# Optimization experiments

Hardware: AMD Instinct MI355X
Metric: run time of the kernel (lower is better)

## Reference

```python
import jax, jax.numpy as jnp
import numpy as np

B, L, E, H = 4, 2048, 1024, 16
D = E // H  # head_dim = 64

def setup_inputs() -> dict:
    key = jax.random.key(0)
    ks = jax.random.split(key, 8)
    s = 1.0 / np.sqrt(E)
    return {
        "x_q": jax.random.normal(ks[0], (B, L, E), jnp.float32),
        "x_k": jax.random.normal(ks[1], (B, L, E), jnp.float32),
        "x_v": jax.random.normal(ks[2], (B, L, E), jnp.float32),
        "Wq": jax.random.uniform(ks[3], (E, E), jnp.float32, -s, s),
        "Wk": jax.random.uniform(ks[4], (E, E), jnp.float32, -s, s),
        "Wv": jax.random.uniform(ks[5], (E, E), jnp.float32, -s, s),
        "Wo": jax.random.uniform(ks[6], (E, E), jnp.float32, -s, s),
        "bo": jax.random.uniform(ks[7], (E,), jnp.float32, -s, s),
    }

def reference(x_q, x_k, x_v, Wq, Wk, Wv, Wo, bo):
    # projections (torch Linear: y = x @ W.T)
    Q = (x_q @ Wq.T).reshape(B, L, H, D).transpose(0, 2, 1, 3)  # (B,H,Lq,D)
    K = (x_k @ Wk.T).reshape(B, L, H, D).transpose(0, 2, 1, 3)
    V = (x_v @ Wv.T).reshape(B, L, H, D).transpose(0, 2, 1, 3)
    scale = 1.0 / jnp.sqrt(jnp.asarray(D, Q.dtype))
    scores = jnp.einsum('bhqd,bhkd->bhqk', Q, K) * scale  # (B,H,Lq,Lk)
    attn = jax.nn.softmax(scores, axis=-1)
    ctx = jnp.einsum('bhqk,bhkd->bhqd', attn, V)
    ctx = ctx.transpose(0, 2, 1, 3).reshape(B, L, E)
    return ctx @ Wo.T + bo
```

## Files before the change

### kernel.cpp

```cpp
#include <hip/hip_runtime.h>
#include <hip/hip_bf16.h>
#include <stdint.h>

typedef __bf16 bf16;
typedef __attribute__((ext_vector_type(8))) __bf16 bf16x8;
typedef __attribute__((ext_vector_type(4))) __bf16 bf16x4;
typedef __attribute__((ext_vector_type(4))) float f32x4;
typedef __attribute__((ext_vector_type(16))) float f32x16;
typedef __attribute__((ext_vector_type(4))) unsigned int u32x4;

#define MFMA(a, b, c) __builtin_amdgcn_mfma_f32_16x16x32_bf16(a, b, c, 0, 0, 0)
#define MFMA32(a, b, c) __builtin_amdgcn_mfma_f32_32x32x16_bf16(a, b, c, 0, 0, 0)

__device__ __forceinline__ void gload16(const void* g, void* l) {
  __builtin_amdgcn_global_load_lds(
      (const __attribute__((address_space(1))) void*)g,
      (__attribute__((address_space(3))) void*)l, 16, 0, 0);
}

__global__ void cvt4(const float* __restrict__ s0, const float* __restrict__ s1,
                     const float* __restrict__ s2, const float* __restrict__ s3,
                     bf16* __restrict__ d0, bf16* __restrict__ d1,
                     bf16* __restrict__ d2, bf16* __restrict__ d3, long n) {
  const float* s = blockIdx.y == 0 ? s0 : blockIdx.y == 1 ? s1 : blockIdx.y == 2 ? s2 : s3;
  bf16* d       = blockIdx.y == 0 ? d0 : blockIdx.y == 1 ? d1 : blockIdx.y == 2 ? d2 : d3;
  long i0 = ((long)blockIdx.x * blockDim.x + threadIdx.x) * 8;
  long gs = (long)gridDim.x * blockDim.x * 8;
  for (long i = i0; i < n; i += gs) {
    float4 a = *(const float4*)(s + i);
    float4 b = *(const float4*)(s + i + 4);
    bf16x8 ov;
    ov[0] = (bf16)a.x; ov[1] = (bf16)a.y; ov[2] = (bf16)a.z; ov[3] = (bf16)a.w;
    ov[4] = (bf16)b.x; ov[5] = (bf16)b.y; ov[6] = (bf16)b.z; ov[7] = (bf16)b.w;
    *(bf16x8*)(d + i) = ov;
  }
}

__device__ __forceinline__ void gemm_body(const bf16* __restrict__ A,
                                          const bf16* __restrict__ W,
                                          void* __restrict__ Cout,
                                          const float* __restrict__ bias,
                                          float scale, int mode,
                                          bf16* As, bf16* Bs) {
  const int tid = threadIdx.x;
  const int l = tid & 63, w = tid >> 6;
  const int lr = l & 15, lg = l >> 4;
  const int lin = blockIdx.y * 8 + blockIdx.x;
  const int nl = (lin & 7) * 64 + (lin >> 3);
  const int m0 = (nl >> 3) * 128, n0 = (nl & 7) * 128;
  const int wm = w >> 1, wn = w & 1;
  f32x4 acc[4][4];
  for (int i = 0; i < 4; i++)
    for (int j = 0; j < 4; j++)
      for (int r = 0; r < 4; r++) acc[i][j][r] = 0.f;

  auto STAGE = [&](int kt, int buf) {
#pragma unroll
    for (int i = 0; i < 2; i++) {
      int c = i * 256 + tid;
      int row = c >> 2, ch = c & 3;
      int sc = (ch ^ ((row >> 1) & 3)) * 8;
      gload16(A + (long)(m0 + row) * 1024 + kt + sc, (char*)As + buf * 8192 + c * 16);
      gload16(W + (long)(n0 + row) * 1024 + kt + sc, (char*)Bs + buf * 8192 + c * 16);
    }
  };

  STAGE(0, 0); STAGE(32, 1); STAGE(64, 2);

  for (int t = 0; t < 32; t++) {
    if (t <= 29)      asm volatile("s_waitcnt vmcnt(8) lgkmcnt(0)" ::: "memory");
    else if (t == 30) asm volatile("s_waitcnt vmcnt(4) lgkmcnt(0)" ::: "memory");
    else              asm volatile("s_waitcnt vmcnt(0) lgkmcnt(0)" ::: "memory");
    __builtin_amdgcn_s_barrier();
    __builtin_amdgcn_sched_barrier(0);
    const char* Ac = (const char*)As + (t & 3) * 8192;
    const char* Bc = (const char*)Bs + (t & 3) * 8192;
    bf16x8 af[4], bw[4];
#pragma unroll
    for (int i = 0; i < 4; i++) {
      int row = wm * 64 + i * 16 + lr;
      af[i] = *(const bf16x8*)(Ac + row * 64 + ((lg ^ ((row >> 1) & 3)) << 4));
    }
#pragma unroll
    for (int j = 0; j < 4; j++) {
      int row = wn * 64 + j * 16 + lr;
      bw[j] = *(const bf16x8*)(Bc + row * 64 + ((lg ^ ((row >> 1) & 3)) << 4));
    }
#pragma unroll
    for (int i = 0; i < 4; i++)
#pragma unroll
      for (int j = 0; j < 4; j++)
        acc[i][j] = MFMA(af[i], bw[j], acc[i][j]);
    if (t <= 28) STAGE((t + 3) * 32, (t + 3) & 3);
  }

  for (int i = 0; i < 4; i++)
    for (int j = 0; j < 4; j++) {
      int row = m0 + wm * 64 + i * 16 + lg * 4;
      int col = n0 + wn * 64 + j * 16 + lr;
      f32x4 v = acc[i][j];
      if (mode == 2) {
        float* O = (float*)Cout;
        float bb = bias[col];
        for (int r = 0; r < 4; r++) O[(long)(row + r) * 1024 + col] = v[r] + bb;
      } else if (mode == 0) {
        bf16* O = (bf16*)Cout;
        for (int r = 0; r < 4; r++) {
          int rr = row + r;
          long idx = ((long)((rr >> 11) * 16 + (col >> 6)) * 2048 + (rr & 2047)) * 64 + (col & 63);
          O[idx] = (bf16)(v[r] * scale);
        }
      } else {
        bf16* O = (bf16*)Cout;
        long idx = ((long)((row >> 11) * 16 + (col >> 6)) * 64 + (col & 63)) * 2048 + (row & 2047);
        bf16x4 pk;
        for (int r = 0; r < 4; r++) pk[r] = (bf16)v[r];
        *(bf16x4*)(O + idx) = pk;
      }
    }
}

__global__ __launch_bounds__(256) void gemm_qkv(const bf16* __restrict__ Xb,
                                                const bf16* __restrict__ Wb,
                                                bf16* __restrict__ Ob,
                                                float qscale) {
  __shared__ bf16 As[4][128 * 32];
  __shared__ bf16 Bs[4][128 * 32];
  const int z = blockIdx.z;
  const bf16* A = Xb + (long)z * 8192 * 1024;
  const bf16* W = Wb + (long)z * 1024 * 1024;
  bf16* O = Ob + (long)z * 8192 * 1024;
  const float scale = (z == 0) ? qscale : 1.0f;
  const int mode = (z == 2) ? 1 : 0;
  gemm_body(A, W, O, nullptr, scale, mode, &As[0][0], &Bs[0][0]);
}

__global__ __launch_bounds__(256) void gemm_out(const bf16* __restrict__ A,
                                                const bf16* __restrict__ W,
                                                float* __restrict__ Cout,
                                                const float* __restrict__ bias) {
  __shared__ bf16 As[4][128 * 32];
  __shared__ bf16 Bs[4][128 * 32];
  gemm_body(A, W, Cout, bias, 1.0f, 2, &As[0][0], &Bs[0][0]);
}

__global__ __launch_bounds__(512, 4) void attn_fwd(const bf16* __restrict__ Q,
                                                   const bf16* __restrict__ K,
                                                   const bf16* __restrict__ Vt,
                                                   bf16* __restrict__ ctx) {
  __shared__ bf16 Ks[2][128 * 64];
  __shared__ bf16 Vs[2][64 * 128];
  const int tid = threadIdx.x;
  const int l = tid & 63, w = tid >> 6;
  const int q32 = l & 31, hl = l >> 5;
  const int lin = blockIdx.y * 8 + blockIdx.x;
  const int nl = (lin & 7) * 64 + (lin >> 3);
  const int bh = nl >> 3, qt = nl & 7;
  const bf16* Qh = Q + (long)bh * 2048 * 64;
  const bf16* Kh = K + (long)bh * 2048 * 64;
  const bf16* Vh = Vt + (long)bh * 64 * 2048;
  const int qb = qt * 256 + w * 32;

#define STAGE(kv0, buf)                                                          \
  {                                                                              \
    _Pragma("unroll") for (int i = 0; i < 2; i++) {                              \
      int c = i * 512 + tid;                                                     \
      int kr = c >> 3, kc = c & 7;                                               \
      gload16(Kh + (long)((kv0) + kr) * 64 + ((kc ^ (kr & 7)) << 3),             \
              (char*)Ks[buf] + c * 16);                                          \
    }                                                                            \
    _Pragma("unroll") for (int i = 0; i < 2; i++) {                              \
      int c = i * 512 + tid;                                                     \
      int r = c >> 4, v0 = c & 15;                                               \
      int vc = (v0 & 8) | ((v0 & 7) ^ (r & 7));                                  \
      gload16(Vh + (long)r * 2048 + (kv0) + vc * 8,                              \
              (char*)Vs[buf] + c * 16);                                          \
    }                                                                            \
  }

  bf16x8 bq[4];
#pragma unroll
  for (int kk = 0; kk < 4; kk++)
    bq[kk] = *(const bf16x8*)(Qh + (long)(qb + q32) * 64 + kk * 16 + hl * 8);

  f32x16 o0, o1;
#pragma unroll
  for (int r = 0; r < 16; r++) { o0[r] = 0.f; o1[r] = 0.f; }
  float lrun = 0.f;

  STAGE(0, 0);
  __syncthreads();

  for (int t = 0; t < 16; t++) {
    const int cur = t & 1;
    if (t < 15) STAGE((t + 1) * 128, cur ^ 1);
    const bf16* Kc = Ks[cur];
    const bf16* Vc = Vs[cur];
    f32x4 psum = {0.f, 0.f, 0.f, 0.f};

#pragma unroll
    for (int nn = 0; nn < 4; nn++) {
      const int row = nn * 32 + q32;
      f32x16 acc;
#pragma unroll
      for (int r = 0; r < 16; r++) acc[r] = 0.f;
      __builtin_amdgcn_s_setprio(1);
#pragma unroll
      for (int kk = 0; kk < 4; kk++) {
        int ch = (kk * 2 + hl) ^ (row & 7);
        bf16x8 ak = *(const bf16x8*)((const char*)Kc + row * 128 + (ch << 4));
        acc = MFMA32(ak, bq[kk], acc);
      }
      __builtin_amdgcn_s_setprio(0);

      f32x16 p;
#pragma unroll
      for (int r = 0; r < 16; r++) p[r] = __builtin_amdgcn_exp2f(acc[r]);
      f32x4 t4;
#pragma unroll
      for (int j = 0; j < 4; j++) t4[j] = (p[j] + p[4 + j]) + (p[8 + j] + p[12 + j]);
      psum += t4;

      unsigned wd[8];
#pragma unroll
      for (int i = 0; i < 8; i++) {
        float lo = p[2 * i], hi = p[2 * i + 1];
        asm("v_cvt_pk_bf16_f32 %0, %1, %2" : "=v"(wd[i]) : "v"(lo), "v"(hi));
      }
#pragma unroll
      for (int ss = 0; ss < 2; ss++) {
        unsigned a0 = wd[ss * 4 + 0], b0 = wd[ss * 4 + 2];
        unsigned a1 = wd[ss * 4 + 1], b1 = wd[ss * 4 + 3];
        asm("v_permlane32_swap_b32 %0, %1" : "+v"(a0), "+v"(b0));
        asm("v_permlane32_swap_b32 %0, %1" : "+v"(a1), "+v"(b1));
        u32x4 pw = {a0, a1, b0, b1};
        bf16x8 bp = *(bf16x8*)&pw;
        int ch0 = (nn * 2 + ss) * 2 + hl;
        __builtin_amdgcn_s_setprio(1);
#pragma unroll
        for (int nd = 0; nd < 2; nd++) {
          int vrw = nd * 32 + q32;
          int ch = (ch0 & 8) | ((ch0 & 7) ^ (vrw & 7));
          bf16x8 av = *(const bf16x8*)((const char*)Vc + vrw * 256 + (ch << 4));
          if (nd == 0) o0 = MFMA32(av, bp, o0);
          else         o1 = MFMA32(av, bp, o1);
        }
        __builtin_amdgcn_s_setprio(0);
      }
    }
    lrun += (psum[0] + psum[1]) + (psum[2] + psum[3]);
    __syncthreads();
  }

  lrun += __shfl_xor(lrun, 32);
  const int b = bh >> 4, h = bh & 15;
  const float inv = 1.0f / lrun;
  const int q = qb + q32;
#pragma unroll
  for (int nd = 0; nd < 2; nd++)
#pragma unroll
    for (int qd = 0; qd < 4; qd++) {
      bf16x4 pk;
#pragma unroll
      for (int r = 0; r < 4; r++)
        pk[r] = (bf16)((nd == 0 ? o0[qd * 4 + r] : o1[qd * 4 + r]) * inv);
      int d = nd * 32 + qd * 8 + hl * 4;
      *(bf16x4*)(ctx + ((long)b * 2048 + q) * 1024 + h * 64 + d) = pk;
    }
#undef STAGE
}

extern "C" void kernel_launch(void* const* d_in, const int* in_sizes, int n_in,
                              void* d_out, int out_size, void* d_ws, size_t ws_size,
                              hipStream_t stream) {
  const float* xq = (const float*)d_in[0];
  const float* xk = (const float*)d_in[1];
  const float* xv = (const float*)d_in[2];
  const float* Wq = (const float*)d_in[3];
  const float* Wk = (const float*)d_in[4];
  const float* Wv = (const float*)d_in[5];
  const float* Wo = (const float*)d_in[6];
  const float* bo = (const float*)d_in[7];

  char* p = (char*)d_ws;
  const size_t SZ_X = (size_t)8192 * 1024 * 2;
  const size_t SZ_W = (size_t)1024 * 1024 * 2;
  bf16* xqb = (bf16*)p; p += SZ_X;
  bf16* xkb = (bf16*)p; p += SZ_X;
  bf16* xvb = (bf16*)p; p += SZ_X;
  bf16* wqb = (bf16*)p; p += SZ_W;
  bf16* wkb = (bf16*)p; p += SZ_W;
  bf16* wvb = (bf16*)p; p += SZ_W;
  bf16* wob = (bf16*)p; p += SZ_W;
  bf16* Qb  = (bf16*)p; p += SZ_X;
  bf16* Kb  = (bf16*)p; p += SZ_X;
  bf16* Vtb = (bf16*)p; p += SZ_X;
  bf16* ctxb = (bf16*)p; p += SZ_X;
  (void)ws_size; (void)in_sizes; (void)n_in; (void)out_size;

  const float QSCALE = 0.18033688011112042f;

  cvt4<<<dim3(1024, 3), 256, 0, stream>>>(xq, xk, xv, xq, xqb, xkb, xvb, xqb,
                                          (long)8192 * 1024);
  cvt4<<<dim3(128, 4), 256, 0, stream>>>(Wq, Wk, Wv, Wo, wqb, wkb, wvb, wob,
                                         (long)1024 * 1024);
  gemm_qkv<<<dim3(8, 64, 3), 256, 0, stream>>>(xqb, wqb, Qb, QSCALE);
  attn_fwd<<<dim3(8, 64), 512, 0, stream>>>(Qb, Kb, Vtb, ctxb);
  gemm_out<<<dim3(8, 64), 256, 0, stream>>>(ctxb, wob, (float*)d_out, bo);
}
```

Baseline: 200.6 us.

## Fuse fp32-to-bf16 activation conversion into QKV GEMM loads

Drops the separate conversion pass over x_q/x_k/x_v. The QKV GEMM now streams fp32 activations straight into LDS with a new XOR swizzle and converts them to bf16 when reading fragments. The pipeline drops from 4 to 3 LDS stages to fit the larger fp32 tiles. This removes a full read+write pass over 3x32MB of activations, but doubles A-tile global and LDS traffic per GEMM, adds conversion ALU work, and shortens prefetch depth.

```diff
diff --git a/kernel.cpp b/kernel.cpp
--- a/kernel.cpp
+++ b/kernel.cpp
@@ -36,64 +36,10 @@
   }
 }
 
-__device__ __forceinline__ void gemm_body(const bf16* __restrict__ A,
-                                          const bf16* __restrict__ W,
-                                          void* __restrict__ Cout,
-                                          const float* __restrict__ bias,
-                                          float scale, int mode,
-                                          bf16* As, bf16* Bs) {
-  const int tid = threadIdx.x;
-  const int l = tid & 63, w = tid >> 6;
-  const int lr = l & 15, lg = l >> 4;
-  const int lin = blockIdx.y * 8 + blockIdx.x;
-  const int nl = (lin & 7) * 64 + (lin >> 3);
-  const int m0 = (nl >> 3) * 128, n0 = (nl & 7) * 128;
-  const int wm = w >> 1, wn = w & 1;
-  f32x4 acc[4][4];
-  for (int i = 0; i < 4; i++)
-    for (int j = 0; j < 4; j++)
-      for (int r = 0; r < 4; r++) acc[i][j][r] = 0.f;
-
-  auto STAGE = [&](int kt, int buf) {
-#pragma unroll
-    for (int i = 0; i < 2; i++) {
-      int c = i * 256 + tid;
-      int row = c >> 2, ch = c & 3;
-      int sc = (ch ^ ((row >> 1) & 3)) * 8;
-      gload16(A + (long)(m0 + row) * 1024 + kt + sc, (char*)As + buf * 8192 + c * 16);
-      gload16(W + (long)(n0 + row) * 1024 + kt + sc, (char*)Bs + buf * 8192 + c * 16);
-    }
-  };
-
-  STAGE(0, 0); STAGE(32, 1); STAGE(64, 2);
-
-  for (int t = 0; t < 32; t++) {
-    if (t <= 29)      asm volatile("s_waitcnt vmcnt(8) lgkmcnt(0)" ::: "memory");
-    else if (t == 30) asm volatile("s_waitcnt vmcnt(4) lgkmcnt(0)" ::: "memory");
-    else              asm volatile("s_waitcnt vmcnt(0) lgkmcnt(0)" ::: "memory");
-    __builtin_amdgcn_s_barrier();
-    __builtin_amdgcn_sched_barrier(0);
-    const char* Ac = (const char*)As + (t & 3) * 8192;
-    const char* Bc = (const char*)Bs + (t & 3) * 8192;
-    bf16x8 af[4], bw[4];
-#pragma unroll
-    for (int i = 0; i < 4; i++) {
-      int row = wm * 64 + i * 16 + lr;
-      af[i] = *(const bf16x8*)(Ac + row * 64 + ((lg ^ ((row >> 1) & 3)) << 4));
-    }
-#pragma unroll
-    for (int j = 0; j < 4; j++) {
-      int row = wn * 64 + j * 16 + lr;
-      bw[j] = *(const bf16x8*)(Bc + row * 64 + ((lg ^ ((row >> 1) & 3)) << 4));
-    }
-#pragma unroll
-    for (int i = 0; i < 4; i++)
-#pragma unroll
-      for (int j = 0; j < 4; j++)
-        acc[i][j] = MFMA(af[i], bw[j], acc[i][j]);
-    if (t <= 28) STAGE((t + 3) * 32, (t + 3) & 3);
-  }
-
+__device__ __forceinline__ void gemm_epilogue(f32x4 (&acc)[4][4], void* Cout,
+                                              const float* bias, float scale,
+                                              int mode, int m0, int n0, int wm,
+                                              int wn, int lr, int lg) {
   for (int i = 0; i < 4; i++)
     for (int j = 0; j < 4; j++) {
       int row = m0 + wm * 64 + i * 16 + lg * 4;
@@ -120,19 +66,87 @@
     }
 }
 
-__global__ __launch_bounds__(256) void gemm_qkv(const bf16* __restrict__ Xb,
+__global__ __launch_bounds__(256) void gemm_qkv(const float* __restrict__ xq,
+                                                const float* __restrict__ xk,
+                                                const float* __restrict__ xv,
                                                 const bf16* __restrict__ Wb,
                                                 bf16* __restrict__ Ob,
                                                 float qscale) {
-  __shared__ bf16 As[4][128 * 32];
-  __shared__ bf16 Bs[4][128 * 32];
+  __shared__ float As[3][128 * 32];
+  __shared__ bf16 Bs[3][128 * 32];
   const int z = blockIdx.z;
-  const bf16* A = Xb + (long)z * 8192 * 1024;
+  const float* A = z == 0 ? xq : (z == 1 ? xk : xv);
   const bf16* W = Wb + (long)z * 1024 * 1024;
   bf16* O = Ob + (long)z * 8192 * 1024;
   const float scale = (z == 0) ? qscale : 1.0f;
   const int mode = (z == 2) ? 1 : 0;
-  gemm_body(A, W, O, nullptr, scale, mode, &As[0][0], &Bs[0][0]);
+
+  const int tid = threadIdx.x;
+  const int l = tid & 63, w = tid >> 6;
+  const int lr = l & 15, lg = l >> 4;
+  const int lin = blockIdx.y * 8 + blockIdx.x;
+  const int nl = (lin & 7) * 64 + (lin >> 3);
+  const int m0 = (nl >> 3) * 128, n0 = (nl & 7) * 128;
+  const int wm = w >> 1, wn = w & 1;
+  f32x4 acc[4][4];
+  for (int i = 0; i < 4; i++)
+    for (int j = 0; j < 4; j++)
+      for (int r = 0; r < 4; r++) acc[i][j][r] = 0.f;
+
+  auto STAGE = [&](int kt, int buf) {
+#pragma unroll
+    for (int i = 0; i < 4; i++) {
+      int c = i * 256 + tid;
+      int row = c >> 3, ch = c & 7;
+      int g = ch ^ (row & 7);
+      gload16(A + (long)(m0 + row) * 1024 + kt + g * 4, (char*)As[buf] + c * 16);
+    }
+#pragma unroll
+    for (int i = 0; i < 2; i++) {
+      int c = i * 256 + tid;
+      int row = c >> 2, ch = c & 3;
+      int g = ch ^ ((row >> 1) & 3);
+      gload16(W + (long)(n0 + row) * 1024 + kt + g * 8, (char*)Bs[buf] + c * 16);
+    }
+  };
+
+  STAGE(0, 0);
+  STAGE(32, 1);
+
+  for (int t = 0; t < 32; t++) {
+    if (t < 31) asm volatile("s_waitcnt vmcnt(6) lgkmcnt(0)" ::: "memory");
+    else        asm volatile("s_waitcnt vmcnt(0) lgkmcnt(0)" ::: "memory");
+    __builtin_amdgcn_s_barrier();
+    __builtin_amdgcn_sched_barrier(0);
+    const int rb = t % 3;
+    const char* Ac = (const char*)As[rb];
+    const char* Bc = (const char*)Bs[rb];
+    bf16x8 af[4], bw[4];
+#pragma unroll
+    for (int i = 0; i < 4; i++) {
+      int row = wm * 64 + i * 16 + lr;
+      const char* base = Ac + row * 128;
+      f32x4 lo = *(const f32x4*)(base + (((2 * lg) ^ (row & 7)) << 4));
+      f32x4 hi = *(const f32x4*)(base + (((2 * lg + 1) ^ (row & 7)) << 4));
+      bf16x8 v;
+      v[0] = (bf16)lo[0]; v[1] = (bf16)lo[1]; v[2] = (bf16)lo[2]; v[3] = (bf16)lo[3];
+      v[4] = (bf16)hi[0]; v[5] = (bf16)hi[1]; v[6] = (bf16)hi[2]; v[7] = (bf16)hi[3];
+      af[i] = v;
+    }
+#pragma unroll
+    for (int j = 0; j < 4; j++) {
+      int row = wn * 64 + j * 16 + lr;
+      bw[j] = *(const bf16x8*)(Bc + row * 64 + ((lg ^ ((row >> 1) & 3)) << 4));
+    }
+#pragma unroll
+    for (int i = 0; i < 4; i++)
+#pragma unroll
+      for (int j = 0; j < 4; j++)
+        acc[i][j] = MFMA(af[i], bw[j], acc[i][j]);
+    if (t <= 29) STAGE((t + 2) * 32, (t + 2) % 3);
+  }
+
+  gemm_epilogue(acc, O, nullptr, scale, mode, m0, n0, wm, wn, lr, lg);
 }
 
 __global__ __launch_bounds__(256) void gemm_out(const bf16* __restrict__ A,
@@ -141,7 +155,59 @@
                                                 const float* __restrict__ bias) {
   __shared__ bf16 As[4][128 * 32];
   __shared__ bf16 Bs[4][128 * 32];
-  gemm_body(A, W, Cout, bias, 1.0f, 2, &As[0][0], &Bs[0][0]);
+  const int tid = threadIdx.x;
+  const int l = tid & 63, w = tid >> 6;
+  const int lr = l & 15, lg = l >> 4;
+  const int lin = blockIdx.y * 8 + blockIdx.x;
+  const int nl = (lin & 7) * 64 + (lin >> 3);
+  const int m0 = (nl >> 3) * 128, n0 = (nl & 7) * 128;
+  const int wm = w >> 1, wn = w & 1;
+  f32x4 acc[4][4];
+  for (int i = 0; i < 4; i++)
+    for (int j = 0; j < 4; j++)
+      for (int r = 0; r < 4; r++) acc[i][j][r] = 0.f;
+
+  auto STAGE = [&](int kt, int buf) {
+#pragma unroll
+    for (int i = 0; i < 2; i++) {
+      int c = i * 256 + tid;
+      int row = c >> 2, ch = c & 3;
+      int sc = (ch ^ ((row >> 1) & 3)) * 8;
+      gload16(A + (long)(m0 + row) * 1024 + kt + sc, (char*)As[0] + buf * 8192 + c * 16);
+      gload16(W + (long)(n0 + row) * 1024 + kt + sc, (char*)Bs[0] + buf * 8192 + c * 16);
+    }
+  };
+
+  STAGE(0, 0); STAGE(32, 1); STAGE(64, 2);
+
+  for (int t = 0; t < 32; t++) {
+    if (t <= 29)      asm volatile("s_waitcnt vmcnt(8) lgkmcnt(0)" ::: "memory");
+    else if (t == 30) asm volatile("s_waitcnt vmcnt(4) lgkmcnt(0)" ::: "memory");
+    else              asm volatile("s_waitcnt vmcnt(0) lgkmcnt(0)" ::: "memory");
+    __builtin_amdgcn_s_barrier();
+    __builtin_amdgcn_sched_barrier(0);
+    const char* Ac = (const char*)As[0] + (t & 3) * 8192;
+    const char* Bc = (const char*)Bs[0] + (t & 3) * 8192;
+    bf16x8 af[4], bw[4];
+#pragma unroll
+    for (int i = 0; i < 4; i++) {
+      int row = wm * 64 + i * 16 + lr;
+      af[i] = *(const bf16x8*)(Ac + row * 64 + ((lg ^ ((row >> 1) & 3)) << 4));
+    }
+#pragma unroll
+    for (int j = 0; j < 4; j++) {
+      int row = wn * 64 + j * 16 + lr;
+      bw[j] = *(const bf16x8*)(Bc + row * 64 + ((lg ^ ((row >> 1) & 3)) << 4));
+    }
+#pragma unroll
+    for (int i = 0; i < 4; i++)
+#pragma unroll
+      for (int j = 0; j < 4; j++)
+        acc[i][j] = MFMA(af[i], bw[j], acc[i][j]);
+    if (t <= 28) STAGE((t + 3) * 32, (t + 3) & 3);
+  }
+
+  gemm_epilogue(acc, Cout, bias, 1.0f, 2, m0, n0, wm, wn, lr, lg);
 }
 
 __global__ __launch_bounds__(512, 4) void attn_fwd(const bf16* __restrict__ Q,
@@ -285,9 +351,6 @@
   char* p = (char*)d_ws;
   const size_t SZ_X = (size_t)8192 * 1024 * 2;
   const size_t SZ_W = (size_t)1024 * 1024 * 2;
-  bf16* xqb = (bf16*)p; p += SZ_X;
-  bf16* xkb = (bf16*)p; p += SZ_X;
-  bf16* xvb = (bf16*)p; p += SZ_X;
   bf16* wqb = (bf16*)p; p += SZ_W;
   bf16* wkb = (bf16*)p; p += SZ_W;
   bf16* wvb = (bf16*)p; p += SZ_W;
@@ -300,11 +363,9 @@
 
   const float QSCALE = 0.18033688011112042f;
 
-  cvt4<<<dim3(1024, 3), 256, 0, stream>>>(xq, xk, xv, xq, xqb, xkb, xvb, xqb,
-                                          (long)8192 * 1024);
   cvt4<<<dim3(128, 4), 256, 0, stream>>>(Wq, Wk, Wv, Wo, wqb, wkb, wvb, wob,
                                          (long)1024 * 1024);
-  gemm_qkv<<<dim3(8, 64, 3), 256, 0, stream>>>(xqb, wqb, Qb, QSCALE);
+  gemm_qkv<<<dim3(8, 64, 3), 256, 0, stream>>>(xq, xk, xv, wqb, Qb, QSCALE);
   attn_fwd<<<dim3(8, 64), 512, 0, stream>>>(Qb, Kb, Vtb, ctxb);
   gemm_out<<<dim3(8, 64), 256, 0, stream>>>(ctxb, wob, (float*)d_out, bo);
 }
```

Result: faster. 193.8 us (-3.4%).
